# Optimization experiments

Measured on AMD Instinct MI355X. Metric: run time of the kernel, lower is better.

Reference implementation:

```python
import jax, jax.numpy as jnp
import numpy as np

N, E, G = 50000, 640000, 128
IN_DIM, LAT, H, HID, NC = 128, 32, 8, 128, 2


def setup_inputs() -> dict:
    key = jax.random.key(0)
    ks = jax.random.split(key, 16)
    x = jax.random.normal(ks[0], (N, IN_DIM), dtype=jnp.float32)
    edge_index = jax.random.randint(ks[1], (2, E), 0, N, dtype=jnp.int64)
    # contiguous graph blocks covering all G graph ids
    batch = (jnp.arange(N, dtype=jnp.int64) * G) // N
    y = jax.random.randint(ks[2], (G,), 0, NC, dtype=jnp.int64)

    def lin(k, fi, fo):
        return jax.random.normal(k, (fi, fo), dtype=jnp.float32) / np.sqrt(fi)

    return {
        'x': x, 'edge_index': edge_index, 'batch': batch, 'y': y,
        'W1': lin(ks[3], IN_DIM, LAT), 'b1': jnp.zeros((LAT,), jnp.float32),
        'Wg1': lin(ks[4], LAT, H * LAT),
        'asrc1': jax.random.normal(ks[5], (H, LAT), jnp.float32) / np.sqrt(LAT),
        'adst1': jax.random.normal(ks[6], (H, LAT), jnp.float32) / np.sqrt(LAT),
        'bg1': jnp.zeros((H * LAT,), jnp.float32),
        'Wg2': lin(ks[7], H * LAT, H * LAT),
        'asrc2': jax.random.normal(ks[8], (H, LAT), jnp.float32) / np.sqrt(LAT),
        'adst2': jax.random.normal(ks[9], (H, LAT), jnp.float32) / np.sqrt(LAT),
        'bg2': jnp.zeros((H * LAT,), jnp.float32),
        'Wl1': lin(ks[10], LAT + 2 * H * LAT, HID), 'bl1': jnp.zeros((HID,), jnp.float32),
        'Wl2': lin(ks[11], HID, NC), 'bl2': jnp.zeros((NC,), jnp.float32),
    }


def _add_self_loops(edge_index, n):
    loop = jnp.arange(n, dtype=edge_index.dtype)
    row = jnp.concatenate([edge_index[0], loop])
    col = jnp.concatenate([edge_index[1], loop])
    return row, col


def gcn_conv(x, row, col, W, b):
    h = x @ W  # [N, C]
    deg = jax.ops.segment_sum(jnp.ones_like(col, dtype=h.dtype), col, num_segments=N)
    dinv = jax.lax.rsqrt(jnp.maximum(deg, 1.0))  # self-loops guarantee deg >= 1
    norm = dinv[row] * dinv[col]  # [E']
    return jax.ops.segment_sum(norm[:, None] * h[row], col, num_segments=N) + b


def gat_conv(x, row, col, W, a_src, a_dst, b):
    h = (x @ W).reshape(N, H, LAT)  # [N, H, C]
    s = jnp.einsum('nhc,hc->nh', h, a_src)
    d = jnp.einsum('nhc,hc->nh', h, a_dst)
    logits = jax.nn.leaky_relu(s[row] + d[col], negative_slope=0.2)  # [E', H]
    m = jax.ops.segment_max(logits, col, num_segments=N)
    m = jnp.where(jnp.isfinite(m), m, 0.0)
    e = jnp.exp(logits - m[col])
    z = jax.ops.segment_sum(e, col, num_segments=N)
    alpha = e / (z[col] + 1e-16)  # segment softmax over incoming edges
    out = jax.ops.segment_sum(alpha[:, :, None] * h[row], col, num_segments=N)
    return out.reshape(N, H * LAT) + b


def reference(x, edge_index, batch, y, W1, b1, Wg1, asrc1, adst1, bg1,
              Wg2, asrc2, adst2, bg2, Wl1, bl1, Wl2, bl2):
    row, col = _add_self_loops(edge_index, N)
    h1 = jax.nn.elu(gcn_conv(x, row, col, W1, b1))
    h2 = jax.nn.elu(gat_conv(h1, row, col, Wg1, asrc1, adst1, bg1))
    h3 = jax.nn.elu(gat_conv(h2, row, col, Wg2, asrc2, adst2, bg2))
    cat = jnp.concatenate([h1, h2, h3], axis=1)  # [N, 544]
    # first node of each graph (batch is sorted, contiguous blocks)
    idx = jnp.searchsorted(batch, jnp.arange(G, dtype=batch.dtype))
    feature = cat[idx] @ Wl1 + bl1  # [G, HID]
    hidden = jax.nn.elu(feature)  # eval mode: dropout off
    raw = hidden @ Wl2 + bl2
    prob = jax.nn.softmax(raw, axis=1)
    logits = jax.nn.log_softmax(raw, axis=1)
    loss = -jnp.mean(jnp.take_along_axis(logits, y[:, None], axis=1))
    pred = jnp.argmax(logits, axis=1, keepdims=True)
    return logits, loss, pred, prob, feature
```

## Files before the change

### kernel.cpp

```cpp
#include <hip/hip_runtime.h>
#include <math.h>

#define NN 50000
#define EE 640000
#define EP (EE + NN)
#define GG 128
#define IND 128
#define LATC 32
#define HH 8
#define HLC 256
#define HIDN 128
#define SCAN_B 256
#define SCAN_G ((NN + SCAN_B - 1) / SCAN_B)

typedef unsigned short ushortT;
typedef unsigned int uintT;
typedef short bf16x8 __attribute__((ext_vector_type(8)));
typedef float f32x4 __attribute__((ext_vector_type(4)));

__device__ __forceinline__ float elu1(float v) { return v > 0.f ? v : (__expf(v) - 1.f); }

__device__ __forceinline__ ushortT f2bf(float f) {
  unsigned int u = __float_as_uint(f);
  return (ushortT)((u + 0x7fffu + ((u >> 16) & 1u)) >> 16);
}
__device__ __forceinline__ float bf2f(ushortT s) {
  return __uint_as_float(((unsigned int)s) << 16);
}

__global__ void count_kernel(const int* col, int* cnt) {
  int t = blockIdx.x * blockDim.x + threadIdx.x;
  if (t < EE) atomicAdd(&cnt[col[t]], 1);
}

__global__ void scan_part_kernel(const int* __restrict__ cnt,
                                 int* __restrict__ bsum) {
  int t = threadIdx.x;
  int i = blockIdx.x * SCAN_B + t;
  int v = (i < NN) ? cnt[i] + 1 : 0;
#pragma unroll
  for (int d = 1; d < 64; d <<= 1) v += __shfl_xor(v, d);
  __shared__ int ws[4];
  if ((t & 63) == 0) ws[t >> 6] = v;
  __syncthreads();
  if (t == 0) bsum[blockIdx.x] = ws[0] + ws[1] + ws[2] + ws[3];
}

__global__ void scan_top_kernel(const int* __restrict__ bsum,
                                int* __restrict__ ebsum,
                                int* __restrict__ offs_last) {
  int t = threadIdx.x;
  int v = (t < SCAN_G) ? bsum[t] : 0;
  int orig = v;
  int lane = t & 63, w = t >> 6;
#pragma unroll
  for (int d = 1; d < 64; d <<= 1) {
    int o = __shfl_up(v, d);
    if (lane >= d) v += o;
  }
  __shared__ int ws[4];
  if (lane == 63) ws[w] = v;
  __syncthreads();
  int add = 0;
  for (int j = 0; j < w; ++j) add += ws[j];
  v += add;
  if (t < SCAN_G) ebsum[t] = v - orig;
  if (t == SCAN_G - 1) *offs_last = v;
}

__global__ void scan_final_kernel(const int* __restrict__ cnt,
                                  const int* __restrict__ ebsum,
                                  int* __restrict__ offs,
                                  float* __restrict__ dinv) {
  int t = threadIdx.x;
  int i = blockIdx.x * SCAN_B + t;
  int v = (i < NN) ? cnt[i] + 1 : 0;
  int orig = v;
  int lane = t & 63, w = t >> 6;
#pragma unroll
  for (int d = 1; d < 64; d <<= 1) {
    int o = __shfl_up(v, d);
    if (lane >= d) v += o;
  }
  __shared__ int ws[4];
  if (lane == 63) ws[w] = v;
  __syncthreads();
  int add = ebsum[blockIdx.x];
  for (int j = 0; j < w; ++j) add += ws[j];
  if (i < NN) {
    offs[i] = v - orig + add;
    dinv[i] = 1.f / sqrtf((float)orig);
  }
}

__global__ void build_kernel(const int* row, const int* col, const int* offs,
                             int* cursor, int* srcs) {
  int t = blockIdx.x * blockDim.x + threadIdx.x;
  if (t >= EP) return;
  int r, c;
  if (t < EE) { r = row[t]; c = col[t]; } else { r = t - EE; c = r; }
  int pos = offs[c] + atomicAdd(&cursor[c], 1);
  srcs[pos] = r;
}

__global__ void finalize_kernel(const int* offs, int* srcs) {
  int gw = (blockIdx.x * blockDim.x + threadIdx.x) >> 6;
  if (gw >= NN) return;
  int lane = threadIdx.x & 63;
  int beg = offs[gw], end = offs[gw + 1];
  int deg = end - beg;
  if (deg <= 64) {
    int v = (lane < deg) ? srcs[beg + lane] : 0x7fffffff;
    for (int k = 2; k <= 64; k <<= 1)
      for (int j = k >> 1; j > 0; j >>= 1) {
        int o = __shfl_xor(v, j);
        bool keepmin = (((lane & k) == 0) == ((lane & j) == 0));
        v = keepmin ? (v < o ? v : o) : (v > o ? v : o);
      }
    if (lane < deg) srcs[beg + lane] = v;
  } else if (lane == 0) {
    for (int i = beg + 1; i < end; ++i) {
      int v = srcs[i]; int j = i - 1;
      while (j >= beg && srcs[j] > v) { srcs[j + 1] = srcs[j]; --j; }
      srcs[j + 1] = v;
    }
  }
}

__launch_bounds__(256)
__global__ void gemm_in_kernel(const float* __restrict__ A,
                               const float* __restrict__ W,
                               float* __restrict__ out) {
  __shared__ float As[32][264];
  __shared__ float Bs[32][32];
  int bm = blockIdx.x * 256;
  int tid = threadIdx.x;
  int tx = tid & 7, ty = tid >> 3;
  float acc[8][4] = {};
  for (int k0 = 0; k0 < IND; k0 += 32) {
    {
      int gm = bm + tid;
      bool ok = gm < NN;
#pragma unroll
      for (int j = 0; j < 8; ++j) {
        float4 v = ok ? *(const float4*)(A + (size_t)gm * IND + k0 + j * 4)
                      : make_float4(0.f, 0.f, 0.f, 0.f);
        As[j * 4 + 0][tid] = v.x; As[j * 4 + 1][tid] = v.y;
        As[j * 4 + 2][tid] = v.z; As[j * 4 + 3][tid] = v.w;
      }
    }
#pragma unroll
    for (int j = 0; j < 4; ++j) {
      int idx = tid + j * 256;
      int kk = idx >> 5, c = idx & 31;
      Bs[kk][c] = W[(size_t)(k0 + kk) * LATC + c];
    }
    __syncthreads();
#pragma unroll 4
    for (int kk = 0; kk < 32; ++kk) {
      float4 a0 = *(const float4*)(&As[kk][ty * 8]);
      float4 a1 = *(const float4*)(&As[kk][ty * 8 + 4]);
      float4 b = *(const float4*)(&Bs[kk][tx * 4]);
      float ar[8] = {a0.x, a0.y, a0.z, a0.w, a1.x, a1.y, a1.z, a1.w};
      float bc[4] = {b.x, b.y, b.z, b.w};
#pragma unroll
      for (int i = 0; i < 8; ++i)
#pragma unroll
        for (int j = 0; j < 4; ++j) acc[i][j] += ar[i] * bc[j];
    }
    __syncthreads();
  }
#pragma unroll
  for (int i = 0; i < 8; ++i) {
    int gm = bm + ty * 8 + i;
    if (gm < NN)
      *(float4*)(out + (size_t)gm * LATC + tx * 4) =
          make_float4(acc[i][0], acc[i][1], acc[i][2], acc[i][3]);
  }
}

__global__ void wsplit_kernel(const float* __restrict__ Wg2,
                              ushortT* __restrict__ WhT,
                              ushortT* __restrict__ WlT) {
  int idx = blockIdx.x * 256 + threadIdx.x;
  if (idx >= HLC * HLC) return;
  int k = idx >> 8, n = idx & 255;
  float f = Wg2[idx];
  ushortT hi = f2bf(f);
  WhT[n * HLC + k] = hi;
  WlT[n * HLC + k] = f2bf(f - bf2f(hi));
}

__launch_bounds__(256)
__global__ void gemm_gat2_mfma(const float* __restrict__ A,
                               const ushortT* __restrict__ WhT,
                               const ushortT* __restrict__ WlT,
                               const float* __restrict__ asrc,
                               const float* __restrict__ adst,
                               ushortT* __restrict__ hgb,
                               float* __restrict__ sbuf,
                               float* __restrict__ dbuf) {
  __shared__ __align__(16) char smem[51200];
  ushortT* Ah = (ushortT*)smem;
  ushortT* Al = Ah + 64 * 40;
  ushortT* Bh = (ushortT*)(smem + 10240);
  ushortT* Bl = Bh + 256 * 40;
  float* LDSf = (float*)(smem + 10240);

  int tid = threadIdx.x;
  int lane = tid & 63;
  int w = tid >> 6;
  int l15 = lane & 15, lg = lane >> 4;
  int bm = blockIdx.x * 64;

  f32x4 zero4 = {0.f, 0.f, 0.f, 0.f};
  f32x4 acc[4][4];
#pragma unroll
  for (int mi = 0; mi < 4; ++mi)
#pragma unroll
    for (int ni = 0; ni < 4; ++ni) acc[mi][ni] = zero4;

  for (int k0 = 0; k0 < HLC; k0 += 32) {
    {
      int row = tid >> 2, kb = (tid & 3) * 8;
      int gm = bm + row;
      float f[8];
      if (gm < NN) {
        float4 u0 = *(const float4*)(A + (size_t)gm * HLC + k0 + kb);
        float4 u1 = *(const float4*)(A + (size_t)gm * HLC + k0 + kb + 4);
        f[0] = u0.x; f[1] = u0.y; f[2] = u0.z; f[3] = u0.w;
        f[4] = u1.x; f[5] = u1.y; f[6] = u1.z; f[7] = u1.w;
      } else {
#pragma unroll
        for (int j = 0; j < 8; ++j) f[j] = 0.f;
      }
      bf16x8 vh, vl;
#pragma unroll
      for (int j = 0; j < 8; ++j) {
        ushortT hi = f2bf(f[j]);
        vh[j] = (short)hi;
        vl[j] = (short)f2bf(f[j] - bf2f(hi));
      }
      *(bf16x8*)(Ah + row * 40 + kb) = vh;
      *(bf16x8*)(Al + row * 40 + kb) = vl;
    }
    {
      const bf16x8* ph = (const bf16x8*)(WhT + (size_t)tid * HLC + k0);
      const bf16x8* pl = (const bf16x8*)(WlT + (size_t)tid * HLC + k0);
#pragma unroll
      for (int i = 0; i < 4; ++i) {
        *(bf16x8*)(Bh + tid * 40 + i * 8) = ph[i];
        *(bf16x8*)(Bl + tid * 40 + i * 8) = pl[i];
      }
    }
    __syncthreads();
    bf16x8 ah[4], al[4], bh[4], bl[4];
#pragma unroll
    for (int mi = 0; mi < 4; ++mi) {
      int off = (mi * 16 + l15) * 40 + lg * 8;
      ah[mi] = *(const bf16x8*)(Ah + off);
      al[mi] = *(const bf16x8*)(Al + off);
    }
#pragma unroll
    for (int ni = 0; ni < 4; ++ni) {
      int off = (w * 64 + ni * 16 + l15) * 40 + lg * 8;
      bh[ni] = *(const bf16x8*)(Bh + off);
      bl[ni] = *(const bf16x8*)(Bl + off);
    }
#pragma unroll
    for (int mi = 0; mi < 4; ++mi)
#pragma unroll
      for (int ni = 0; ni < 4; ++ni) {
        acc[mi][ni] = __builtin_amdgcn_mfma_f32_16x16x32_bf16(
            al[mi], bh[ni], acc[mi][ni], 0, 0, 0);
        acc[mi][ni] = __builtin_amdgcn_mfma_f32_16x16x32_bf16(
            ah[mi], bl[ni], acc[mi][ni], 0, 0, 0);
        acc[mi][ni] = __builtin_amdgcn_mfma_f32_16x16x32_bf16(
            ah[mi], bh[ni], acc[mi][ni], 0, 0, 0);
      }
    __syncthreads();
  }

  float av[4], bv[4];
#pragma unroll
  for (int ni = 0; ni < 4; ++ni) {
    int c = w * 64 + ni * 16 + l15;
    av[ni] = asrc[c];
    bv[ni] = adst[c];
  }
#pragma unroll
  for (int mi = 0; mi < 4; ++mi)
#pragma unroll
    for (int r = 0; r < 4; ++r) {
      int gm = bm + mi * 16 + lg * 4 + r;
      float s0 = acc[mi][0][r] * av[0] + acc[mi][1][r] * av[1];
      float s1 = acc[mi][2][r] * av[2] + acc[mi][3][r] * av[3];
      float d0 = acc[mi][0][r] * bv[0] + acc[mi][1][r] * bv[1];
      float d1 = acc[mi][2][r] * bv[2] + acc[mi][3][r] * bv[3];
#pragma unroll
      for (int m = 1; m <= 8; m <<= 1) {
        s0 += __shfl_xor(s0, m);
        s1 += __shfl_xor(s1, m);
        d0 += __shfl_xor(d0, m);
        d1 += __shfl_xor(d1, m);
      }
      if (l15 == 0 && gm < NN) {
        sbuf[gm * HH + 2 * w] = s0;
        sbuf[gm * HH + 2 * w + 1] = s1;
        dbuf[gm * HH + 2 * w] = d0;
        dbuf[gm * HH + 2 * w + 1] = d1;
      }
    }

#pragma unroll
  for (int p = 0; p < 2; ++p) {
    __syncthreads();
#pragma unroll
    for (int q = 0; q < 2; ++q) {
      int mi = 2 * p + q;
#pragma unroll
      for (int ni = 0; ni < 4; ++ni)
#pragma unroll
        for (int r = 0; r < 4; ++r) {
          int lrow = q * 16 + lg * 4 + r;
          LDSf[lrow * 260 + w * 64 + ni * 16 + l15] = acc[mi][ni][r];
        }
    }
    __syncthreads();
    int row = tid >> 3, cb = (tid & 7) * 32;
    int gm = bm + p * 32 + row;
    if (gm < NN) {
      uintT u[16];
#pragma unroll
      for (int i = 0; i < 8; ++i) {
        float4 v = *(const float4*)(LDSf + row * 260 + cb + i * 4);
        u[2 * i] = (uintT)f2bf(v.x) | ((uintT)f2bf(v.y) << 16);
        u[2 * i + 1] = (uintT)f2bf(v.z) | ((uintT)f2bf(v.w) << 16);
      }
      uintT* dst = (uintT*)(hgb + (size_t)gm * HLC + cb);
#pragma unroll
      for (int i = 0; i < 4; ++i) {
        uint4 s;
        s.x = u[4 * i]; s.y = u[4 * i + 1];
        s.z = u[4 * i + 2]; s.w = u[4 * i + 3];
        *(uint4*)(dst + 4 * i) = s;
      }
    }
  }
}

__global__ void gcn_agg_kernel(const float* __restrict__ hW, const int* offs,
                               const int* srcs, const float* dinv,
                               const float* b1, float* h1) {
  int wid = (blockIdx.x * blockDim.x + threadIdx.x) >> 6;
  if (wid >= NN) return;
  int lane = threadIdx.x & 63;
  int c = lane & 31, half = lane >> 5;
  int beg = offs[wid], end = offs[wid + 1];
  float acc = 0.f;
  for (int p = beg + half; p < end; p += 2) {
    int src = srcs[p];
    acc += dinv[src] * hW[src * LATC + c];
  }
  acc += __shfl_xor(acc, 32);
  if (lane < 32) {
    float v = dinv[wid] * acc + b1[c];
    h1[wid * LATC + c] = elu1(v);
  }
}

__global__ void sd1_kernel(const float* __restrict__ h1,
                           const float* __restrict__ Wg1,
                           const float* __restrict__ asrc,
                           const float* __restrict__ adst, float* s,
                           float* d) {
  __shared__ float va[HLC], vb[HLC];
  int t = threadIdx.x;
  {
    int c = t & 31, h = t >> 5;
    float sa = 0.f, sb = 0.f;
#pragma unroll 8
    for (int j = 0; j < 32; ++j) {
      float w = Wg1[(size_t)c * HLC + h * 32 + j];
      sa += w * asrc[h * 32 + j];
      sb += w * adst[h * 32 + j];
    }
    va[t] = sa;
    vb[t] = sb;
  }
  __syncthreads();
  int idx = blockIdx.x * 256 + t;
  if (idx >= NN * HH) return;
  int n = idx >> 3, h = idx & 7;
  const float4* hv = (const float4*)(h1 + (size_t)n * LATC);
  const float4* av = (const float4*)(va + h * LATC);
  const float4* bv = (const float4*)(vb + h * LATC);
  float ss = 0.f, dd = 0.f;
#pragma unroll
  for (int i = 0; i < 8; ++i) {
    float4 xx = hv[i], aa = av[i], bb = bv[i];
    ss += xx.x * aa.x + xx.y * aa.y + xx.z * aa.z + xx.w * aa.w;
    dd += xx.x * bb.x + xx.y * bb.y + xx.z * bb.z + xx.w * bb.w;
  }
  s[idx] = ss; d[idx] = dd;
}

__global__ void gat1_agg_kernel(const float* __restrict__ h1,
                                const float* __restrict__ s,
                                const float* __restrict__ dd, const int* offs,
                                const int* srcs, float* __restrict__ agg) {
  int wid = (blockIdx.x * blockDim.x + threadIdx.x) >> 6;
  if (wid >= NN) return;
  int lane = threadIdx.x & 63;
  int g = lane >> 5;
  int l5 = lane & 31;
  int h = l5 >> 2;
  int c8 = (l5 & 3) * 8;
  int beg = offs[wid], end = offs[wid + 1];
  float dn = dd[wid * HH + h];
  float self = s[wid * HH + h] + dn;
  float m = self > 0.f ? self : 0.2f * self;
  float z = 0.f;
  float a[8] = {};
#pragma unroll 2
  for (int p = beg + g; p < end; p += 2) {
    int src = srcs[p];
    float sv = s[src * HH + h] + dn;
    float logit = sv > 0.f ? sv : 0.2f * sv;
    float e = __expf(logit - m);
    z += e;
    float4 v0 = *(const float4*)(h1 + (size_t)src * LATC + c8);
    float4 v1 = *(const float4*)(h1 + (size_t)src * LATC + c8 + 4);
    a[0] += e * v0.x; a[1] += e * v0.y; a[2] += e * v0.z; a[3] += e * v0.w;
    a[4] += e * v1.x; a[5] += e * v1.y; a[6] += e * v1.z; a[7] += e * v1.w;
  }
  z += __shfl_xor(z, 32);
#pragma unroll
  for (int j = 0; j < 8; ++j) a[j] += __shfl_xor(a[j], 32);
  if (g == 0) {
    float zinv = 1.f / (z + 1e-16f);
    *(float4*)(agg + (size_t)wid * HLC + h * LATC + c8) =
        make_float4(a[0] * zinv, a[1] * zinv, a[2] * zinv, a[3] * zinv);
    *(float4*)(agg + (size_t)wid * HLC + h * LATC + c8 + 4) =
        make_float4(a[4] * zinv, a[5] * zinv, a[6] * zinv, a[7] * zinv);
  }
}

__launch_bounds__(256)
__global__ void gat1_proj_kernel(const float* __restrict__ agg,
                                 const float* __restrict__ Wg1,
                                 const float* __restrict__ bg,
                                 float* __restrict__ h2) {
  __shared__ float As[HLC][32];
  __shared__ float Ws[32][HLC];
  int bm = blockIdx.x * 32;
  int t = threadIdx.x;
  {
    const float4* Wv = (const float4*)Wg1;
    float4* Bv = (float4*)Ws;
#pragma unroll
    for (int i = 0; i < 8; ++i) Bv[t + i * 256] = Wv[t + i * 256];
  }
  {
    int n = t & 31, cb = (t >> 5) * 32;
    int gm = bm + n;
#pragma unroll
    for (int j = 0; j < 8; ++j) {
      float4 v = make_float4(0.f, 0.f, 0.f, 0.f);
      if (gm < NN) v = *(const float4*)(agg + (size_t)gm * HLC + cb + j * 4);
      As[cb + j * 4 + 0][n] = v.x;
      As[cb + j * 4 + 1][n] = v.y;
      As[cb + j * 4 + 2][n] = v.z;
      As[cb + j * 4 + 3][n] = v.w;
    }
  }
  __syncthreads();
  int tx = t & 31, ty = t >> 5;
  int h1o = (tx >> 3) * 32;
  int h2o = 128 + (tx >> 3) * 32;
  float acc1[4][4] = {}, acc2[4][4] = {};
#pragma unroll 4
  for (int kk = 0; kk < 32; ++kk) {
    float4 a1 = *(const float4*)(&As[h1o + kk][ty * 4]);
    float4 a2 = *(const float4*)(&As[h2o + kk][ty * 4]);
    float4 w1 = *(const float4*)(&Ws[kk][tx * 4]);
    float4 w2 = *(const float4*)(&Ws[kk][128 + tx * 4]);
    float ar1[4] = {a1.x, a1.y, a1.z, a1.w};
    float ar2[4] = {a2.x, a2.y, a2.z, a2.w};
    float wr1[4] = {w1.x, w1.y, w1.z, w1.w};
    float wr2[4] = {w2.x, w2.y, w2.z, w2.w};
#pragma unroll
    for (int r = 0; r < 4; ++r)
#pragma unroll
      for (int q = 0; q < 4; ++q) {
        acc1[r][q] += ar1[r] * wr1[q];
        acc2[r][q] += ar2[r] * wr2[q];
      }
  }
  float4 b1 = *(const float4*)(bg + tx * 4);
  float4 b2 = *(const float4*)(bg + 128 + tx * 4);
  float bb1[4] = {b1.x, b1.y, b1.z, b1.w};
  float bb2[4] = {b2.x, b2.y, b2.z, b2.w};
#pragma unroll
  for (int r = 0; r < 4; ++r) {
    int gm = bm + ty * 4 + r;
    if (gm >= NN) continue;
    float4 o1, o2;
    o1.x = elu1(acc1[r][0] + bb1[0]); o1.y = elu1(acc1[r][1] + bb1[1]);
    o1.z = elu1(acc1[r][2] + bb1[2]); o1.w = elu1(acc1[r][3] + bb1[3]);
    o2.x = elu1(acc2[r][0] + bb2[0]); o2.y = elu1(acc2[r][1] + bb2[1]);
    o2.z = elu1(acc2[r][2] + bb2[2]); o2.w = elu1(acc2[r][3] + bb2[3]);
    *(float4*)(h2 + (size_t)gm * HLC + tx * 4) = o1;
    *(float4*)(h2 + (size_t)gm * HLC + 128 + tx * 4) = o2;
  }
}

__global__ void gat_agg_kernel(const ushortT* __restrict__ hgb,
                               const float* __restrict__ s,
                               const float* __restrict__ dd, const int* offs,
                               const int* srcs, const float* bg, float* out) {
  int wid = (blockIdx.x * blockDim.x + threadIdx.x) >> 6;
  if (wid >= NN) return;
  int lane = threadIdx.x & 63;
  int hh = lane >> 3;
  int ch = lane << 2;
  int beg = offs[wid], end = offs[wid + 1];
  float dn = dd[wid * HH + hh];
  float self = s[wid * HH + hh] + dn;
  float m = self > 0.f ? self : 0.2f * self;
  float z = 0.f;
  float ax = 0.f, ay = 0.f, az = 0.f, aw = 0.f;
#pragma unroll 4
  for (int p = beg; p < end; ++p) {
    int src = srcs[p];
    float xv = s[src * HH + hh] + dn;
    float logit = xv > 0.f ? xv : 0.2f * xv;
    float e = __expf(logit - m);
    z += e;
    ushort4 v = *(const ushort4*)(hgb + (size_t)src * HLC + ch);
    ax += e * bf2f(v.x); ay += e * bf2f(v.y);
    az += e * bf2f(v.z); aw += e * bf2f(v.w);
  }
  float zinv = 1.f / (z + 1e-16f);
  float4 bb = *(const float4*)(bg + ch);
  float4 o;
  o.x = elu1(ax * zinv + bb.x); o.y = elu1(ay * zinv + bb.y);
  o.z = elu1(az * zinv + bb.z); o.w = elu1(aw * zinv + bb.w);
  *(float4*)(out + (size_t)wid * HLC + ch) = o;
}

__global__ void head_kernel(const float* __restrict__ h1,
                            const float* __restrict__ h2,
                            const float* __restrict__ h3, const int* batch,
                            const int* y, const float* __restrict__ Wl1,
                            const float* bl1, const float* __restrict__ Wl2,
                            const float* bl2, float* out, float* lterms) {
  int g = blockIdx.x, tid = threadIdx.x;
  __shared__ float cat[544];
  __shared__ float hidden[HIDN];
  __shared__ float raw_s[2];
  __shared__ int idx_s;
  if (tid == 0) {
    int lo = 0, hi = NN;
    while (lo < hi) { int mid = (lo + hi) >> 1; if (batch[mid] < g) lo = mid + 1; else hi = mid; }
    idx_s = lo;
  }
  __syncthreads();
  int idx = idx_s;
  if (tid < 32) cat[tid] = h1[idx * LATC + tid];
  for (int i = tid; i < HLC; i += HIDN) {
    cat[32 + i] = h2[(size_t)idx * HLC + i];
    cat[288 + i] = h3[(size_t)idx * HLC + i];
  }
  __syncthreads();
  float f = bl1[tid];
  for (int k = 0; k < 544; ++k) f += cat[k] * Wl1[k * HIDN + tid];
  out[641 + g * HIDN + tid] = f;
  hidden[tid] = elu1(f);
  __syncthreads();
  if (tid < 2) {
    float r = bl2[tid];
    for (int j = 0; j < HIDN; ++j) r += hidden[j] * Wl2[j * 2 + tid];
    raw_s[tid] = r;
  }
  __syncthreads();
  if (tid == 0) {
    float r0 = raw_s[0], r1 = raw_s[1];
    float mx = fmaxf(r0, r1);
    float e0 = expf(r0 - mx), e1 = expf(r1 - mx);
    float zz = e0 + e1;
    float lse = mx + logf(zz);
    float lg0 = r0 - lse, lg1 = r1 - lse;
    out[g * 2 + 0] = lg0; out[g * 2 + 1] = lg1;
    out[385 + g * 2 + 0] = e0 / zz; out[385 + g * 2 + 1] = e1 / zz;
    out[257 + g] = (r1 > r0) ? 1.f : 0.f;
    lterms[g] = -((y[g] == 0) ? lg0 : lg1);
  }
}

__global__ void loss_kernel(const float* lterms, float* out) {
  __shared__ float buf[GG];
  int tid = threadIdx.x;
  buf[tid] = lterms[tid];
  __syncthreads();
  for (int off = GG / 2; off > 0; off >>= 1) {
    if (tid < off) buf[tid] += buf[tid + off];
    __syncthreads();
  }
  if (tid == 0) out[256] = buf[0] / (float)GG;
}

extern "C" void kernel_launch(void* const* d_in, const int* in_sizes, int n_in,
                              void* d_out, int out_size, void* d_ws,
                              size_t ws_size, hipStream_t stream) {
  const float* x = (const float*)d_in[0];
  const int* ei = (const int*)d_in[1];
  const int* batch = (const int*)d_in[2];
  const int* y = (const int*)d_in[3];
  const float* W1 = (const float*)d_in[4];
  const float* b1 = (const float*)d_in[5];
  const float* Wg1 = (const float*)d_in[6];
  const float* asrc1 = (const float*)d_in[7];
  const float* adst1 = (const float*)d_in[8];
  const float* bg1 = (const float*)d_in[9];
  const float* Wg2 = (const float*)d_in[10];
  const float* asrc2 = (const float*)d_in[11];
  const float* adst2 = (const float*)d_in[12];
  const float* bg2 = (const float*)d_in[13];
  const float* Wl1 = (const float*)d_in[14];
  const float* bl1 = (const float*)d_in[15];
  const float* Wl2 = (const float*)d_in[16];
  const float* bl2 = (const float*)d_in[17];
  float* out = (float*)d_out;

  const int* erow = ei;
  const int* ecol = ei + EE;

  char* p = (char*)d_ws;
  auto alloc = [&](size_t bytes) {
    void* r = (void*)p;
    p += (bytes + 255) & ~(size_t)255;
    return r;
  };
  int* cntcur = (int*)alloc((size_t)2 * NN * 4);
  int* cnt = cntcur;
  int* cursor = cntcur + NN;
  int* offs = (int*)alloc((NN + 1) * 4);
  int* srcs = (int*)alloc((size_t)EP * 4);
  int* bsum = (int*)alloc(SCAN_G * 4);
  int* ebsum = (int*)alloc(SCAN_G * 4);
  float* dinv = (float*)alloc(NN * 4);
  float* hW = (float*)alloc((size_t)NN * LATC * 4);
  float* h1 = (float*)alloc((size_t)NN * LATC * 4);
  float* hg = (float*)alloc((size_t)NN * HLC * 4);
  float* h2 = (float*)alloc((size_t)NN * HLC * 4);
  float* h3 = (float*)alloc((size_t)NN * HLC * 4);
  float* sbuf = (float*)alloc((size_t)NN * HH * 4);
  float* dbuf = (float*)alloc((size_t)NN * HH * 4);
  float* lterms = (float*)alloc(GG * 4);
  ushortT* whT = (ushortT*)alloc((size_t)HLC * HLC * 2);
  ushortT* wlT = (ushortT*)alloc((size_t)HLC * HLC * 2);
  ushortT* hgb = (ushortT*)hg;

  const int NBLK = (NN + 63) / 64;

  hipMemsetAsync(cntcur, 0, (size_t)2 * NN * 4, stream);
  count_kernel<<<(EE + 255) / 256, 256, 0, stream>>>(ecol, cnt);
  scan_part_kernel<<<SCAN_G, SCAN_B, 0, stream>>>(cnt, bsum);
  scan_top_kernel<<<1, 256, 0, stream>>>(bsum, ebsum, offs + NN);
  scan_final_kernel<<<SCAN_G, SCAN_B, 0, stream>>>(cnt, ebsum, offs, dinv);
  build_kernel<<<(EP + 255) / 256, 256, 0, stream>>>(erow, ecol, offs, cursor, srcs);
  finalize_kernel<<<(NN + 3) / 4, 256, 0, stream>>>(offs, srcs);

  wsplit_kernel<<<(HLC * HLC + 255) / 256, 256, 0, stream>>>(Wg2, whT, wlT);

  gemm_in_kernel<<<(NN + 255) / 256, 256, 0, stream>>>(x, W1, hW);
  gcn_agg_kernel<<<(NN + 3) / 4, 256, 0, stream>>>(hW, offs, srcs, dinv, b1, h1);

  sd1_kernel<<<(NN * HH + 255) / 256, 256, 0, stream>>>(h1, Wg1, asrc1, adst1,
                                                        sbuf, dbuf);
  gat1_agg_kernel<<<(NN + 3) / 4, 256, 0, stream>>>(h1, sbuf, dbuf, offs, srcs, hg);
  gat1_proj_kernel<<<(NN + 31) / 32, 256, 0, stream>>>(hg, Wg1, bg1, h2);

  gemm_gat2_mfma<<<NBLK, 256, 0, stream>>>(h2, whT, wlT, asrc2, adst2, hgb,
                                           sbuf, dbuf);
  gat_agg_kernel<<<(NN + 3) / 4, 256, 0, stream>>>(hgb, sbuf, dbuf, offs, srcs, bg2, h3);

  head_kernel<<<GG, HIDN, 0, stream>>>(h1, h2, h3, batch, y, Wl1, bl1, Wl2, bl2,
                                       out, lterms);
  loss_kernel<<<1, GG, 0, stream>>>(lterms, out);
}
```

Before: 375.3 us.

## Fuse GCN aggregation with attention scores, GAT1 aggregation with projection, and loss into head

Merges the GCN aggregation and the per-node attention score computation into one kernel, so h1 is not re-read to compute s and d. Fuses GAT layer-1 softmax aggregation with the per-head projection in a persistent grid-stride kernel, so the 50000x256 intermediate aggregate is never written to or read back from global memory. Folds the loss reduction into the head kernel with an atomic ticket, removing one launch. The fused projection now does a per-node matvec from LDS instead of a tiled GEMM, which lowers arithmetic reuse. The gcn_agg_sd kernel also has no bounds check on wid, which is fine only because NN is a multiple of 4.

```diff
diff --git a/kernel.cpp b/kernel.cpp
--- a/kernel.cpp
+++ b/kernel.cpp
@@ -12,6 +12,7 @@
 #define HIDN 128
 #define SCAN_B 256
 #define SCAN_G ((NN + SCAN_B - 1) / SCAN_B)
+#define AGP_BLOCKS 2048
 
 typedef unsigned short ushortT;
 typedef unsigned int uintT;
@@ -349,32 +350,14 @@
   }
 }
 
-__global__ void gcn_agg_kernel(const float* __restrict__ hW, const int* offs,
-                               const int* srcs, const float* dinv,
-                               const float* b1, float* h1) {
-  int wid = (blockIdx.x * blockDim.x + threadIdx.x) >> 6;
-  if (wid >= NN) return;
-  int lane = threadIdx.x & 63;
-  int c = lane & 31, half = lane >> 5;
-  int beg = offs[wid], end = offs[wid + 1];
-  float acc = 0.f;
-  for (int p = beg + half; p < end; p += 2) {
-    int src = srcs[p];
-    acc += dinv[src] * hW[src * LATC + c];
-  }
-  acc += __shfl_xor(acc, 32);
-  if (lane < 32) {
-    float v = dinv[wid] * acc + b1[c];
-    h1[wid * LATC + c] = elu1(v);
-  }
-}
-
-__global__ void sd1_kernel(const float* __restrict__ h1,
-                           const float* __restrict__ Wg1,
-                           const float* __restrict__ asrc,
-                           const float* __restrict__ adst, float* s,
-                           float* d) {
+__global__ void gcn_agg_sd_kernel(const float* __restrict__ hW,
+                                  const int* offs, const int* srcs,
+                                  const float* dinv, const float* b1,
+                                  const float* __restrict__ Wg1,
+                                  const float* asrc, const float* adst,
+                                  float* h1, float* s, float* d) {
   __shared__ float va[HLC], vb[HLC];
+  __shared__ float rowbuf[4][LATC];
   int t = threadIdx.x;
   {
     int c = t & 31, h = t >> 5;
@@ -389,71 +372,49 @@
     vb[t] = sb;
   }
   __syncthreads();
-  int idx = blockIdx.x * 256 + t;
-  if (idx >= NN * HH) return;
-  int n = idx >> 3, h = idx & 7;
-  const float4* hv = (const float4*)(h1 + (size_t)n * LATC);
-  const float4* av = (const float4*)(va + h * LATC);
-  const float4* bv = (const float4*)(vb + h * LATC);
-  float ss = 0.f, dd = 0.f;
-#pragma unroll
-  for (int i = 0; i < 8; ++i) {
-    float4 xx = hv[i], aa = av[i], bb = bv[i];
-    ss += xx.x * aa.x + xx.y * aa.y + xx.z * aa.z + xx.w * aa.w;
-    dd += xx.x * bb.x + xx.y * bb.y + xx.z * bb.z + xx.w * bb.w;
-  }
-  s[idx] = ss; d[idx] = dd;
-}
-
-__global__ void gat1_agg_kernel(const float* __restrict__ h1,
-                                const float* __restrict__ s,
-                                const float* __restrict__ dd, const int* offs,
-                                const int* srcs, float* __restrict__ agg) {
-  int wid = (blockIdx.x * blockDim.x + threadIdx.x) >> 6;
-  if (wid >= NN) return;
-  int lane = threadIdx.x & 63;
-  int g = lane >> 5;
-  int l5 = lane & 31;
-  int h = l5 >> 2;
-  int c8 = (l5 & 3) * 8;
+  int wid = (blockIdx.x * blockDim.x + t) >> 6;
+  int lane = t & 63;
+  int wv = t >> 6;
+  int c = lane & 31, half = lane >> 5;
   int beg = offs[wid], end = offs[wid + 1];
-  float dn = dd[wid * HH + h];
-  float self = s[wid * HH + h] + dn;
-  float m = self > 0.f ? self : 0.2f * self;
-  float z = 0.f;
-  float a[8] = {};
-#pragma unroll 2
-  for (int p = beg + g; p < end; p += 2) {
+  float acc = 0.f;
+  for (int p = beg + half; p < end; p += 2) {
     int src = srcs[p];
-    float sv = s[src * HH + h] + dn;
-    float logit = sv > 0.f ? sv : 0.2f * sv;
-    float e = __expf(logit - m);
-    z += e;
-    float4 v0 = *(const float4*)(h1 + (size_t)src * LATC + c8);
-    float4 v1 = *(const float4*)(h1 + (size_t)src * LATC + c8 + 4);
-    a[0] += e * v0.x; a[1] += e * v0.y; a[2] += e * v0.z; a[3] += e * v0.w;
-    a[4] += e * v1.x; a[5] += e * v1.y; a[6] += e * v1.z; a[7] += e * v1.w;
-  }
-  z += __shfl_xor(z, 32);
-#pragma unroll
-  for (int j = 0; j < 8; ++j) a[j] += __shfl_xor(a[j], 32);
-  if (g == 0) {
-    float zinv = 1.f / (z + 1e-16f);
-    *(float4*)(agg + (size_t)wid * HLC + h * LATC + c8) =
-        make_float4(a[0] * zinv, a[1] * zinv, a[2] * zinv, a[3] * zinv);
-    *(float4*)(agg + (size_t)wid * HLC + h * LATC + c8 + 4) =
-        make_float4(a[4] * zinv, a[5] * zinv, a[6] * zinv, a[7] * zinv);
+    acc += dinv[src] * hW[src * LATC + c];
+  }
+  acc += __shfl_xor(acc, 32);
+  if (lane < 32) {
+    float v = elu1(dinv[wid] * acc + b1[c]);
+    h1[wid * LATC + c] = v;
+    rowbuf[wv][c] = v;
+  }
+  int h = lane >> 3, k = lane & 7;
+  float ps = 0.f, pd = 0.f;
+#pragma unroll
+  for (int j = 0; j < 4; ++j) {
+    float x = rowbuf[wv][k * 4 + j];
+    ps += x * va[h * 32 + k * 4 + j];
+    pd += x * vb[h * 32 + k * 4 + j];
+  }
+  ps += __shfl_xor(ps, 1); pd += __shfl_xor(pd, 1);
+  ps += __shfl_xor(ps, 2); pd += __shfl_xor(pd, 2);
+  ps += __shfl_xor(ps, 4); pd += __shfl_xor(pd, 4);
+  if (k == 0) {
+    s[wid * HH + h] = ps;
+    d[wid * HH + h] = pd;
   }
 }
 
 __launch_bounds__(256)
-__global__ void gat1_proj_kernel(const float* __restrict__ agg,
-                                 const float* __restrict__ Wg1,
-                                 const float* __restrict__ bg,
-                                 float* __restrict__ h2) {
-  __shared__ float As[HLC][32];
+__global__ void gat1_aggproj_kernel(const float* __restrict__ h1,
+                                    const float* __restrict__ s,
+                                    const float* __restrict__ d,
+                                    const int* offs, const int* srcs,
+                                    const float* __restrict__ Wg1,
+                                    const float* __restrict__ bg,
+                                    float* __restrict__ h2) {
   __shared__ float Ws[32][HLC];
-  int bm = blockIdx.x * 32;
+  __shared__ float aggs[4][HLC];
   int t = threadIdx.x;
   {
     const float4* Wv = (const float4*)Wg1;
@@ -461,57 +422,50 @@
 #pragma unroll
     for (int i = 0; i < 8; ++i) Bv[t + i * 256] = Wv[t + i * 256];
   }
-  {
-    int n = t & 31, cb = (t >> 5) * 32;
-    int gm = bm + n;
-#pragma unroll
-    for (int j = 0; j < 8; ++j) {
-      float4 v = make_float4(0.f, 0.f, 0.f, 0.f);
-      if (gm < NN) v = *(const float4*)(agg + (size_t)gm * HLC + cb + j * 4);
-      As[cb + j * 4 + 0][n] = v.x;
-      As[cb + j * 4 + 1][n] = v.y;
-      As[cb + j * 4 + 2][n] = v.z;
-      As[cb + j * 4 + 3][n] = v.w;
-    }
-  }
-  __syncthreads();
-  int tx = t & 31, ty = t >> 5;
-  int h1o = (tx >> 3) * 32;
-  int h2o = 128 + (tx >> 3) * 32;
-  float acc1[4][4] = {}, acc2[4][4] = {};
-#pragma unroll 4
-  for (int kk = 0; kk < 32; ++kk) {
-    float4 a1 = *(const float4*)(&As[h1o + kk][ty * 4]);
-    float4 a2 = *(const float4*)(&As[h2o + kk][ty * 4]);
-    float4 w1 = *(const float4*)(&Ws[kk][tx * 4]);
-    float4 w2 = *(const float4*)(&Ws[kk][128 + tx * 4]);
-    float ar1[4] = {a1.x, a1.y, a1.z, a1.w};
-    float ar2[4] = {a2.x, a2.y, a2.z, a2.w};
-    float wr1[4] = {w1.x, w1.y, w1.z, w1.w};
-    float wr2[4] = {w2.x, w2.y, w2.z, w2.w};
-#pragma unroll
-    for (int r = 0; r < 4; ++r)
-#pragma unroll
-      for (int q = 0; q < 4; ++q) {
-        acc1[r][q] += ar1[r] * wr1[q];
-        acc2[r][q] += ar2[r] * wr2[q];
-      }
-  }
-  float4 b1 = *(const float4*)(bg + tx * 4);
-  float4 b2 = *(const float4*)(bg + 128 + tx * 4);
-  float bb1[4] = {b1.x, b1.y, b1.z, b1.w};
-  float bb2[4] = {b2.x, b2.y, b2.z, b2.w};
-#pragma unroll
-  for (int r = 0; r < 4; ++r) {
-    int gm = bm + ty * 4 + r;
-    if (gm >= NN) continue;
-    float4 o1, o2;
-    o1.x = elu1(acc1[r][0] + bb1[0]); o1.y = elu1(acc1[r][1] + bb1[1]);
-    o1.z = elu1(acc1[r][2] + bb1[2]); o1.w = elu1(acc1[r][3] + bb1[3]);
-    o2.x = elu1(acc2[r][0] + bb2[0]); o2.y = elu1(acc2[r][1] + bb2[1]);
-    o2.z = elu1(acc2[r][2] + bb2[2]); o2.w = elu1(acc2[r][3] + bb2[3]);
-    *(float4*)(h2 + (size_t)gm * HLC + tx * 4) = o1;
-    *(float4*)(h2 + (size_t)gm * HLC + 128 + tx * 4) = o2;
+  __syncthreads();
+  int lane = t & 63;
+  int wv = t >> 6;
+  int g = lane >> 5, l5 = lane & 31;
+  int h = l5 >> 2, c8 = (l5 & 3) * 8;
+  int qb = lane * 4, hq = lane >> 3;
+  float4 bb = *(const float4*)(bg + qb);
+  for (int wid = blockIdx.x * 4 + wv; wid < NN; wid += AGP_BLOCKS * 4) {
+    int beg = offs[wid], end = offs[wid + 1];
+    float dn = d[wid * HH + h];
+    float self = s[wid * HH + h] + dn;
+    float m = self > 0.f ? self : 0.2f * self;
+    float z = 0.f;
+    float a[8] = {};
+#pragma unroll 2
+    for (int p = beg + g; p < end; p += 2) {
+      int src = srcs[p];
+      float sv = s[src * HH + h] + dn;
+      float logit = sv > 0.f ? sv : 0.2f * sv;
+      float e = __expf(logit - m);
+      z += e;
+      float4 v0 = *(const float4*)(h1 + (size_t)src * LATC + c8);
+      float4 v1 = *(const float4*)(h1 + (size_t)src * LATC + c8 + 4);
+      a[0] += e * v0.x; a[1] += e * v0.y; a[2] += e * v0.z; a[3] += e * v0.w;
+      a[4] += e * v1.x; a[5] += e * v1.y; a[6] += e * v1.z; a[7] += e * v1.w;
+    }
+    z += __shfl_xor(z, 32);
+#pragma unroll
+    for (int j = 0; j < 8; ++j) a[j] += __shfl_xor(a[j], 32);
+    float zinv = 1.f / (z + 1e-16f);
+    if (g == 0) {
+#pragma unroll
+      for (int j = 0; j < 8; ++j)
+        aggs[wv][h * 32 + c8 + j] = a[j] * zinv;
+    }
+    float o0 = bb.x, o1 = bb.y, o2 = bb.z, o3 = bb.w;
+#pragma unroll 8
+    for (int cc = 0; cc < 32; ++cc) {
+      float av = aggs[wv][hq * 32 + cc];
+      float4 w4 = *(const float4*)(&Ws[cc][qb]);
+      o0 += av * w4.x; o1 += av * w4.y; o2 += av * w4.z; o3 += av * w4.w;
+    }
+    *(float4*)(h2 + (size_t)wid * HLC + qb) =
+        make_float4(elu1(o0), elu1(o1), elu1(o2), elu1(o3));
   }
 }
 
@@ -554,7 +508,8 @@
                             const float* __restrict__ h3, const int* batch,
                             const int* y, const float* __restrict__ Wl1,
                             const float* bl1, const float* __restrict__ Wl2,
-                            const float* bl2, float* out, float* lterms) {
+                            const float* bl2, float* out, float* lterms,
+                            int* done) {
   int g = blockIdx.x, tid = threadIdx.x;
   __shared__ float cat[544];
   __shared__ float hidden[HIDN];
@@ -595,19 +550,15 @@
     out[385 + g * 2 + 0] = e0 / zz; out[385 + g * 2 + 1] = e1 / zz;
     out[257 + g] = (r1 > r0) ? 1.f : 0.f;
     lterms[g] = -((y[g] == 0) ? lg0 : lg1);
-  }
-}
-
-__global__ void loss_kernel(const float* lterms, float* out) {
-  __shared__ float buf[GG];
-  int tid = threadIdx.x;
-  buf[tid] = lterms[tid];
-  __syncthreads();
-  for (int off = GG / 2; off > 0; off >>= 1) {
-    if (tid < off) buf[tid] += buf[tid + off];
-    __syncthreads();
-  }
-  if (tid == 0) out[256] = buf[0] / (float)GG;
+    __threadfence();
+    int ticket = atomicAdd(done, 1);
+    if (ticket == GG - 1) {
+      __threadfence();
+      float sum = 0.f;
+      for (int j = 0; j < GG; ++j) sum += lterms[j];
+      out[256] = sum / (float)GG;
+    }
+  }
 }
 
 extern "C" void kernel_launch(void* const* d_in, const int* in_sizes, int n_in,
@@ -642,9 +593,10 @@
     p += (bytes + 255) & ~(size_t)255;
     return r;
   };
-  int* cntcur = (int*)alloc((size_t)2 * NN * 4);
+  int* cntcur = (int*)alloc(((size_t)2 * NN + 64) * 4);
   int* cnt = cntcur;
   int* cursor = cntcur + NN;
+  int* done = cntcur + 2 * NN;
   int* offs = (int*)alloc((NN + 1) * 4);
   int* srcs = (int*)alloc((size_t)EP * 4);
   int* bsum = (int*)alloc(SCAN_G * 4);
@@ -664,7 +616,7 @@
 
   const int NBLK = (NN + 63) / 64;
 
-  hipMemsetAsync(cntcur, 0, (size_t)2 * NN * 4, stream);
+  hipMemsetAsync(cntcur, 0, ((size_t)2 * NN + 64) * 4, stream);
   count_kernel<<<(EE + 255) / 256, 256, 0, stream>>>(ecol, cnt);
   scan_part_kernel<<<SCAN_G, SCAN_B, 0, stream>>>(cnt, bsum);
   scan_top_kernel<<<1, 256, 0, stream>>>(bsum, ebsum, offs + NN);
@@ -675,18 +627,16 @@
   wsplit_kernel<<<(HLC * HLC + 255) / 256, 256, 0, stream>>>(Wg2, whT, wlT);
 
   gemm_in_kernel<<<(NN + 255) / 256, 256, 0, stream>>>(x, W1, hW);
-  gcn_agg_kernel<<<(NN + 3) / 4, 256, 0, stream>>>(hW, offs, srcs, dinv, b1, h1);
-
-  sd1_kernel<<<(NN * HH + 255) / 256, 256, 0, stream>>>(h1, Wg1, asrc1, adst1,
-                                                        sbuf, dbuf);
-  gat1_agg_kernel<<<(NN + 3) / 4, 256, 0, stream>>>(h1, sbuf, dbuf, offs, srcs, hg);
-  gat1_proj_kernel<<<(NN + 31) / 32, 256, 0, stream>>>(hg, Wg1, bg1, h2);
+  gcn_agg_sd_kernel<<<(NN + 3) / 4, 256, 0, stream>>>(
+      hW, offs, srcs, dinv, b1, Wg1, asrc1, adst1, h1, sbuf, dbuf);
+
+  gat1_aggproj_kernel<<<AGP_BLOCKS, 256, 0, stream>>>(h1, sbuf, dbuf, offs,
+                                                      srcs, Wg1, bg1, h2);
 
   gemm_gat2_mfma<<<NBLK, 256, 0, stream>>>(h2, whT, wlT, asrc2, adst2, hgb,
                                            sbuf, dbuf);
   gat_agg_kernel<<<(NN + 3) / 4, 256, 0, stream>>>(hgb, sbuf, dbuf, offs, srcs, bg2, h3);
 
-  head_kernel<<<GG, HIDN, 0, stream>>>(h1, h2, h3, batch, y, Wl1, bl1, Wl2, bl2,
-                                       out, lterms);
-  loss_kernel<<<1, GG, 0, stream>>>(lterms, out);
-}
+  head_kernel<<<GG, HIDN, 0, stream>>>(h1, h2, h3, batch, y, Wl1, bl1, Wl2,
+                                       bl2, out, lterms, done);
+}
```

Measured after the change: 407.0 us. 1.08x slower.
